# Kernel optimization log

Measured on AMD Instinct MI355X. Metric: run time of the kernel, lower is better.

The kernel has to match this reference:

```python
import jax, jax.numpy as jnp
import numpy as np

B, T, H = 2, 2048, 1024
I = 4096            # intermediate dim
HEADS = 4
RET = 128           # private expert retrieval dim
NUM_EXPERTS = 4096
NUM_KEYS = 64       # sqrt(NUM_EXPERTS)
K = 8               # num_cdmmoe_experts_per_head


def setup_inputs() -> dict:
    key = jax.random.key(0)
    ks = jax.random.split(key, 7)
    return {
        "hidden_states": jax.random.normal(ks[0], (B, T, H), jnp.float32),
        "W_up": jax.random.normal(ks[1], (I, H), jnp.float32) * 0.02,
        "W_down": jax.random.normal(ks[2], (H, I), jnp.float32) * 0.02,
        "W_q": jax.random.normal(ks[3], (HEADS * RET, H), jnp.float32) * 0.02,
        "keys": jax.random.normal(ks[4], (HEADS, NUM_KEYS, 2, RET // 2), jnp.float32) * 0.02,
        "down_embed": jax.random.normal(ks[5], (NUM_EXPERTS, H), jnp.float32) * 0.02,
        "up_embed": jax.random.normal(ks[6], (NUM_EXPERTS, H), jnp.float32) * 0.02,
    }


def reference(hidden_states, W_up, W_down, W_q, keys, down_embed, up_embed):
    b, t, hd = hidden_states.shape
    h, nk, _, n = keys.shape  # heads, num_keys, 2, half retrieval dim
    # queries: [b,t,h*2n] -> [2,b,t,h,n]
    q = jnp.einsum('btd,ed->bte', hidden_states, W_q)
    q = q.reshape(b, t, 2, h, n).transpose(2, 0, 1, 3, 4)
    # product-key similarities: [2,b,t,h,num_keys]
    sim = jnp.einsum('pbthn,hkpn->pbthk', q, keys)
    scores_xy, idx_xy = jax.lax.top_k(sim, K)  # [2,b,t,h,K]
    sx, sy = scores_xy[0], scores_xy[1]
    ix, iy = idx_xy[0], idx_xy[1]
    # cartesian combine: [b,t,h,K*K]
    all_scores = (sx[..., :, None] + sy[..., None, :]).reshape(b, t, h, K * K)
    all_idx = (ix[..., :, None] * nk + iy[..., None, :]).reshape(b, t, h, K * K)
    scores, pk = jax.lax.top_k(all_scores, K)               # [b,t,h,K]
    indices = jnp.take_along_axis(all_idx, pk, axis=-1)     # [b,t,h,K]
    de = down_embed[indices]  # [b,t,h,K,H]
    ue = up_embed[indices]    # [b,t,h,K,H]
    w = jax.nn.silu(jnp.einsum('btd,bthkd->bthk', hidden_states, de)
                    * jax.nn.softmax(scores, axis=-1))
    experts_states = jnp.einsum('bthk,bthkd->btd', w, ue)
    dense = jnp.einsum('bti,di->btd', jax.nn.silu(jnp.einsum('btd,id->bti', hidden_states, W_up)), W_down)
    return dense + experts_states
```

## Files before the change

### kernel.cpp

```cpp
#include <hip/hip_runtime.h>

typedef unsigned short u16;
typedef unsigned int u32;

#define TOKENS 4096
#define HDIM 1024
#define IDIM 4096
#define NHEADS 4
#define NKEYS 64
#define TOPK 8
#define QDIM 512

typedef __bf16 bf16x8 __attribute__((ext_vector_type(8)));
typedef float  f32x4  __attribute__((ext_vector_type(4)));
typedef u16    u16x8  __attribute__((ext_vector_type(8)));
typedef u32    u32x4  __attribute__((ext_vector_type(4)));

__device__ __forceinline__ u16 f2bf(float f) {
    u32 u = __float_as_uint(f);
    u += 0x7fffu + ((u >> 16) & 1u);
    return (u16)(u >> 16);
}
__device__ __forceinline__ float bf2f(u16 h) { return __uint_as_float(((u32)h) << 16); }

#define H_N4   1048576
#define WUP_N4 1048576
#define WDN_N4 1048576
#define DE_N4  1048576
#define UE_N4  1048576
#define CVT_TOT (H_N4 + WUP_N4)

__device__ __forceinline__ void cvt1(const float* in, u16* hi, u16* lo, int i) {
    float4 v = reinterpret_cast<const float4*>(in)[i];
    float vf[4] = {v.x, v.y, v.z, v.w};
    ushort4 h;
    u16 hh[4];
#pragma unroll
    for (int j = 0; j < 4; j++) hh[j] = f2bf(vf[j]);
    h.x = hh[0]; h.y = hh[1]; h.z = hh[2]; h.w = hh[3];
    reinterpret_cast<ushort4*>(hi)[i] = h;
    if (lo) {
        ushort4 l4;
        u16 ll[4];
#pragma unroll
        for (int j = 0; j < 4; j++) ll[j] = f2bf(vf[j] - bf2f(hh[j]));
        l4.x = ll[0]; l4.y = ll[1]; l4.z = ll[2]; l4.w = ll[3];
        reinterpret_cast<ushort4*>(lo)[i] = l4;
    }
}

__device__ __forceinline__ void cvt1_f8(const float* in, u32* out8, int i) {
    float4 v = reinterpret_cast<const float4*>(in)[i];
    u32 w = __builtin_amdgcn_cvt_pk_fp8_f32(v.x, v.y, 0u, false);
    w = __builtin_amdgcn_cvt_pk_fp8_f32(v.z, v.w, w, true);
    out8[i] = w;
}

__global__ __launch_bounds__(256) void cvt_all(
    const float* __restrict__ hidden, const float* __restrict__ W_up,
    u16* __restrict__ hid_hi, u16* __restrict__ hid_lo, u16* __restrict__ wup) {
    int i = blockIdx.x * 256 + threadIdx.x;
    if (i >= CVT_TOT) return;
    if (i < H_N4) { cvt1(hidden, hid_hi, hid_lo, i); return; }
    i -= H_N4;
    cvt1(W_up, wup, nullptr, i);
}

__global__ __launch_bounds__(256) void weff_kernel(
    const float* __restrict__ keys, const float* __restrict__ Wq,
    u16* __restrict__ weff_hi, u16* __restrict__ weff_lo) {
    __shared__ float kk[64][65];
    __shared__ float wq_s[64][128];

    const int g = blockIdx.x >> 3, ds = blockIdx.x & 7;
    const int p = g >> 2, h = g & 3;
    const int d0 = ds * 128;
    const int t = threadIdx.x;
    const int base = p * 256 + h * 64;

    {
        int k = t >> 2, part = t & 3;
        const float* krow = keys + (((size_t)(h * NKEYS + k) * 2 + p) * 64);
#pragma unroll
        for (int j = 0; j < 4; j++) {
            int n0 = part * 16 + j * 4;
            float4 v = *reinterpret_cast<const float4*>(krow + n0);
            kk[k][n0 + 0] = v.x; kk[k][n0 + 1] = v.y;
            kk[k][n0 + 2] = v.z; kk[k][n0 + 3] = v.w;
        }
    }
    {
        int n = t >> 2, dpart = t & 3;
        const float* wrow = Wq + (size_t)(base + n) * HDIM + d0;
#pragma unroll
        for (int j = 0; j < 8; j++) {
            int dd = dpart * 32 + j * 4;
            float4 v = *reinterpret_cast<const float4*>(wrow + dd);
            *reinterpret_cast<float4*>(&wq_s[n][dd]) = v;
        }
    }
    __syncthreads();

    const int k = t & 63, dq = t >> 6;
    float acc[32];
#pragma unroll
    for (int i = 0; i < 32; i++) acc[i] = 0.f;
    for (int n = 0; n < 64; n++) {
        float kv = kk[k][n];
        const float4* wrow = reinterpret_cast<const float4*>(&wq_s[n][dq * 32]);
#pragma unroll
        for (int j = 0; j < 8; j++) {
            float4 w4 = wrow[j];
            acc[j * 4 + 0] += kv * w4.x; acc[j * 4 + 1] += kv * w4.y;
            acc[j * 4 + 2] += kv * w4.z; acc[j * 4 + 3] += kv * w4.w;
        }
    }
    size_t ro = (size_t)(g * 64 + k) * HDIM + d0 + dq * 32;
#pragma unroll
    for (int j = 0; j < 8; j++) {
        ushort4 hh, ll;
        u16 hv[4], lv[4];
#pragma unroll
        for (int i = 0; i < 4; i++) {
            float a = acc[j * 4 + i];
            hv[i] = f2bf(a);
            lv[i] = f2bf(a - bf2f(hv[i]));
        }
        hh.x = hv[0]; hh.y = hv[1]; hh.z = hv[2]; hh.w = hv[3];
        ll.x = lv[0]; ll.y = lv[1]; ll.z = lv[2]; ll.w = lv[3];
        *reinterpret_cast<ushort4*>(weff_hi + ro + j * 4) = hh;
        *reinterpret_cast<ushort4*>(weff_lo + ro + j * 4) = ll;
    }
}

__global__ __launch_bounds__(256) void reduce_add4(float* __restrict__ out,
                                                   const float* __restrict__ p,
                                                   const float* __restrict__ ea,
                                                   const float* __restrict__ eb, int n4) {
    int i = blockIdx.x * 256 + threadIdx.x;
    if (i >= n4) return;
    float4 a = reinterpret_cast<const float4*>(out)[i];
    float4 b = reinterpret_cast<const float4*>(p)[i];
    float4 c = reinterpret_cast<const float4*>(ea)[i];
    float4 d = reinterpret_cast<const float4*>(eb)[i];
    a.x += b.x + c.x + d.x; a.y += b.y + c.y + d.y;
    a.z += b.z + c.z + d.z; a.w += b.w + c.w + d.w;
    reinterpret_cast<float4*>(out)[i] = a;
}

__device__ __forceinline__ void gload16(const void* g, void* s) {
    auto gp = reinterpret_cast<const __attribute__((address_space(1))) u32*>(
        reinterpret_cast<uintptr_t>(g));
    auto sp = reinterpret_cast<__attribute__((address_space(3))) u32*>(
        reinterpret_cast<uintptr_t>(s));
    __builtin_amdgcn_global_load_lds(gp, sp, 16, 0, 0);
}

#define BK 32

__device__ __forceinline__ int swz(int a) { return a ^ (((a >> 7) & 3) << 4); }

template <int ROWS, int THREADS>
__device__ __forceinline__ void stage_tile(const u16* g, size_t krow_b, size_t kb0,
                                           char* s, int t) {
#pragma unroll
    for (int rnd = 0; rnd < ROWS * 64 / (THREADS * 16); rnd++) {
        int o = t * 16 + rnd * THREADS * 16;
        int os = swz(o);
        int row = o >> 6, kb = os & 63;
        gload16((const char*)g + (size_t)row * krow_b + kb0 + kb, s + o);
    }
}

template <int N>
__device__ __forceinline__ void vm_wait() {
    if constexpr (N == 0) asm volatile("s_waitcnt vmcnt(0)" ::: "memory");
    else if constexpr (N == 3) asm volatile("s_waitcnt vmcnt(3)" ::: "memory");
    else if constexpr (N == 4) asm volatile("s_waitcnt vmcnt(4)" ::: "memory");
    else if constexpr (N == 6) asm volatile("s_waitcnt vmcnt(6)" ::: "memory");
    else if constexpr (N == 8) asm volatile("s_waitcnt vmcnt(8)" ::: "memory");
    else static_assert(N == 0, "unsupported vmcnt");
}

__device__ void up_body(char* smem, int bx, int by,
                        const u16* __restrict__ A, const u16* __restrict__ B,
                        u16* __restrict__ act, int M, int N, int K) {
    constexpr int LPS = 3;
    const int t = threadIdx.x;
    const int lane = t & 63;
    const int wave = t >> 6;
    const int wr = wave >> 1, wc = wave & 1;
    const int ro = lane & 15;
    const int ko = (lane >> 4) * 16;
    const int m0 = by * 256, n0 = bx * 128;

    f32x4 acc[4][4];
#pragma unroll
    for (int i = 0; i < 4; i++)
#pragma unroll
        for (int j = 0; j < 4; j++) acc[i][j] = (f32x4){0.f, 0.f, 0.f, 0.f};

    const size_t krow = (size_t)K * 2;
    const u16* Ab = A + (size_t)m0 * K;
    const u16* Bb = B + (size_t)n0 * K;
    char* smA = smem;
    char* smB = smem + 49152;

    auto stage_all = [&](int b, int k0) {
        size_t kb0 = (size_t)k0 * 2;
        stage_tile<256, 512>(Ab, krow, kb0, smA + b * 16384, t);
        stage_tile<128, 512>(Bb, krow, kb0, smB + b * 8192, t);
    };

    const int NU = K / BK;
    stage_all(0, 0);
    stage_all(1, BK);

    int cur = 0, pre = 2;
    for (int u = 0; u < NU; ++u) {
        if (u + 2 < NU) stage_all(pre, (u + 2) * BK);
        if (u + 2 < NU) vm_wait<2 * LPS>();
        else if (u + 1 < NU) vm_wait<LPS>();
        else vm_wait<0>();
        __builtin_amdgcn_s_barrier();

        const char* Ac = smA + cur * 16384;
        const char* Bc = smB + cur * 8192;
        bf16x8 fa[4], fb[4];
#pragma unroll
        for (int i = 0; i < 4; i++)
            fa[i] = *reinterpret_cast<const bf16x8*>(Ac + swz((wr * 64 + i * 16 + ro) * 64 + ko));
#pragma unroll
        for (int j = 0; j < 4; j++)
            fb[j] = *reinterpret_cast<const bf16x8*>(Bc + swz((wc * 64 + j * 16 + ro) * 64 + ko));
#pragma unroll
        for (int i = 0; i < 4; i++)
#pragma unroll
            for (int j = 0; j < 4; j++)
                acc[i][j] = __builtin_amdgcn_mfma_f32_16x16x32_bf16(fa[i], fb[j],
                                                                    acc[i][j], 0, 0, 0);
        __builtin_amdgcn_s_barrier();
        cur = (cur == 2) ? 0 : cur + 1;
        pre = (pre == 2) ? 0 : pre + 1;
    }

#pragma unroll
    for (int i = 0; i < 4; i++)
#pragma unroll
        for (int j = 0; j < 4; j++) {
            int col = n0 + wc * 64 + j * 16 + ro;
            int rbase = m0 + wr * 64 + i * 16 + (lane >> 4) * 4;
#pragma unroll
            for (int r = 0; r < 4; r++) {
                float v = acc[i][j][r];
                float s = v / (1.f + __expf(-v));
                act[(size_t)(rbase + r) * N + col] = f2bf(s);
            }
        }
}

__device__ void sim_body(char* smem, int bx, int by,
                         const u16* __restrict__ Ahi, const u16* __restrict__ Alo,
                         const u16* __restrict__ Bhi, const u16* __restrict__ Blo,
                         float* __restrict__ C, int M, int N, int K) {
    const int t = threadIdx.x;
    const int lane = t & 63;
    const int wave = t >> 6;
    const int wr = wave >> 2, wc = wave & 3;
    const int ro = lane & 15;
    const int ko = (lane >> 4) * 16;
    const int m0 = by * 64, n0 = bx * 128;

    f32x4 acc[2][2];
#pragma unroll
    for (int i = 0; i < 2; i++)
#pragma unroll
        for (int j = 0; j < 2; j++) acc[i][j] = (f32x4){0.f, 0.f, 0.f, 0.f};

    const size_t krow = (size_t)K * 2;
    const u16* Ahb = Ahi + (size_t)m0 * K;
    const u16* Alb = Alo + (size_t)m0 * K;
    const u16* Bhb = Bhi + (size_t)n0 * K;
    const u16* Blb = Blo + (size_t)n0 * K;
    char* smA = smem;
    char* smB = smem + 16384;

    auto stage_all = [&](int b, int k0) {
        size_t kb0 = (size_t)k0 * 2;
        {
            int sel = t >> 8, tt = t & 255;
            const u16* g = sel ? Alb : Ahb;
            int o = tt * 16;
            int os = swz(o);
            gload16((const char*)g + (size_t)(o >> 6) * krow + kb0 + (os & 63),
                    smA + b * 8192 + sel * 4096 + o);
        }
        {
            int o = t * 16, os = swz(o);
            gload16((const char*)Bhb + (size_t)(o >> 6) * krow + kb0 + (os & 63),
                    smB + b * 16384 + o);
        }
        {
            int o = t * 16, os = swz(o);
            gload16((const char*)Blb + (size_t)(o >> 6) * krow + kb0 + (os & 63),
                    smB + b * 16384 + 8192 + o);
        }
    };

    stage_all(0, 0);
    __syncthreads();
    int cur = 0;

    for (int k0 = 0; k0 < K; k0 += BK) {
        if (k0 + BK < K) stage_all(cur ^ 1, k0 + BK);
        const char* Ac = smA + cur * 8192;
        const char* Bc = smB + cur * 16384;
        bf16x8 fa[2], fal[2], fb[2], fbl[2];
#pragma unroll
        for (int i = 0; i < 2; i++) {
            int a = swz((wr * 32 + i * 16 + ro) * 64 + ko);
            fa[i] = *reinterpret_cast<const bf16x8*>(Ac + a);
            fal[i] = *reinterpret_cast<const bf16x8*>(Ac + 4096 + a);
        }
#pragma unroll
        for (int j = 0; j < 2; j++) {
            int a = swz((wc * 32 + j * 16 + ro) * 64 + ko);
            fb[j] = *reinterpret_cast<const bf16x8*>(Bc + a);
            fbl[j] = *reinterpret_cast<const bf16x8*>(Bc + 8192 + a);
        }
#pragma unroll
        for (int i = 0; i < 2; i++)
#pragma unroll
            for (int j = 0; j < 2; j++) {
                acc[i][j] = __builtin_amdgcn_mfma_f32_16x16x32_bf16(fa[i], fb[j],
                                                                    acc[i][j], 0, 0, 0);
                acc[i][j] = __builtin_amdgcn_mfma_f32_16x16x32_bf16(fa[i], fbl[j],
                                                                    acc[i][j], 0, 0, 0);
                acc[i][j] = __builtin_amdgcn_mfma_f32_16x16x32_bf16(fal[i], fb[j],
                                                                    acc[i][j], 0, 0, 0);
            }
        __syncthreads();
        cur ^= 1;
    }

#pragma unroll
    for (int i = 0; i < 2; i++)
#pragma unroll
        for (int j = 0; j < 2; j++) {
            int col = n0 + wc * 32 + j * 16 + ro;
            int rbase = m0 + wr * 32 + i * 16 + (lane >> 4) * 4;
#pragma unroll
            for (int r = 0; r < 4; r++)
                C[(size_t)(rbase + r) * N + col] = acc[i][j][r];
        }
}

__global__ __launch_bounds__(512, 4) void up_sim(
    const u16* __restrict__ hid_hi, const u16* __restrict__ hid_lo,
    const u16* __restrict__ wup,
    const u16* __restrict__ weff_hi, const u16* __restrict__ weff_lo,
    const float* __restrict__ W_down, const float* __restrict__ de,
    const float* __restrict__ ue,
    u16* __restrict__ act, float* __restrict__ Simb,
    u16* __restrict__ wdn, u32* __restrict__ de_f8, u32* __restrict__ ue_f8) {
    __shared__ char smem[73728];
    int bid = blockIdx.x;
    if (bid < 512) {
        int b2 = (bid & 7) * 64 + (bid >> 3);
        up_body(smem, b2 % 32, b2 / 32, hid_hi, wup, act, TOKENS, IDIM, HDIM);
    } else if (bid < 768) {
        int sb = bid - 512;
        sim_body(smem, sb & 3, sb >> 2, hid_hi, hid_lo, weff_hi, weff_lo, Simb,
                 TOKENS, QDIM, HDIM);
    } else {
        int idx = (bid - 768) * 512 + threadIdx.x;
#pragma unroll
        for (int j = 0; j < 24; j++) {
            int i = idx + j * 131072;
            if (i < WDN_N4) cvt1(W_down, wdn, nullptr, i);
            else if (i < WDN_N4 + DE_N4) cvt1_f8(de, de_f8, i - WDN_N4);
            else cvt1_f8(ue, ue_f8, i - WDN_N4 - DE_N4);
        }
    }
}

template <int TBM, int TBN, int WVM, int WVN, int KCHUNKS>
__global__ __launch_bounds__(WVM * WVN * 64) void gemm_p3(
    const u16* __restrict__ A, const u16* __restrict__ B,
    float* __restrict__ Cout, float* __restrict__ Cout2, int M, int N, int K) {
    constexpr int THREADS = WVM * WVN * 64;
    constexpr int WM = TBM / WVM, WN = TBN / WVN;
    constexpr int FM = WM / 16, FN = WN / 16;
    constexpr int LPS = (TBM + TBN) * 64 / (THREADS * 16);
    __shared__ u16 As[3][TBM * BK];
    __shared__ u16 Bs[3][TBN * BK];
    const int t = threadIdx.x;
    const int lane = t & 63;
    const int wave = t >> 6;
    const int wr = wave / WVN, wc = wave % WVN;
    const int ro = lane & 15;
    const int ko = (lane >> 4) * 16;

    int bx = blockIdx.x, by = blockIdx.y;
    {
        int gx = gridDim.x;
        int n = gx * gridDim.y;
        int bid = by * gx + bx;
        int q = n >> 3;
        bid = (bid & 7) * q + (bid >> 3);
        bx = bid % gx; by = bid / gx;
    }
    const int m0 = by * TBM;
    const int n0 = bx * TBN;
    const int klen = K / KCHUNKS;
    const int z = (KCHUNKS > 1) ? blockIdx.z : 0;
    const int koff = z * klen;
    const int NU = klen / BK;

    f32x4 acc[FM][FN];
#pragma unroll
    for (int i = 0; i < FM; i++)
#pragma unroll
        for (int j = 0; j < FN; j++) acc[i][j] = (f32x4){0.f, 0.f, 0.f, 0.f};

    const size_t krow = (size_t)K * 2;
    const u16* Ab = A + (size_t)m0 * K;
    const u16* Bb = B + (size_t)n0 * K;

    auto stage_all = [&](int b, int k0) {
        size_t kb0 = (size_t)k0 * 2;
        stage_tile<TBM, THREADS>(Ab, krow, kb0, (char*)As[b], t);
        stage_tile<TBN, THREADS>(Bb, krow, kb0, (char*)Bs[b], t);
    };

    stage_all(0, koff);
    stage_all(1, koff + BK);

    int cur = 0, pre = 2;
    for (int u = 0; u < NU; ++u) {
        int k0 = koff + u * BK;
        if (u + 2 < NU) stage_all(pre, k0 + 2 * BK);
        if (u + 2 < NU) vm_wait<2 * LPS>();
        else if (u + 1 < NU) vm_wait<LPS>();
        else vm_wait<0>();
        __builtin_amdgcn_s_barrier();

        const u16* Ac = As[cur];
        const u16* Bc = Bs[cur];
        bf16x8 fa[FM], fb[FN];
#pragma unroll
        for (int i = 0; i < FM; i++)
            fa[i] = *reinterpret_cast<const bf16x8*>(
                (const char*)Ac + swz((wr * WM + i * 16 + ro) * 64 + ko));
#pragma unroll
        for (int j = 0; j < FN; j++)
            fb[j] = *reinterpret_cast<const bf16x8*>(
                (const char*)Bc + swz((wc * WN + j * 16 + ro) * 64 + ko));
#pragma unroll
        for (int i = 0; i < FM; i++)
#pragma unroll
            for (int j = 0; j < FN; j++)
                acc[i][j] = __builtin_amdgcn_mfma_f32_16x16x32_bf16(fa[i], fb[j],
                                                                    acc[i][j], 0, 0, 0);
        __builtin_amdgcn_s_barrier();
        cur = (cur == 2) ? 0 : cur + 1;
        pre = (pre == 2) ? 0 : pre + 1;
    }

#pragma unroll
    for (int i = 0; i < FM; i++)
#pragma unroll
        for (int j = 0; j < FN; j++) {
            int col = n0 + wc * WN + j * 16 + ro;
            int rbase = m0 + wr * WM + i * 16 + (lane >> 4) * 4;
#pragma unroll
            for (int r = 0; r < 4; r++) {
                size_t off = (size_t)(rbase + r) * N + col;
                if (z == 0) Cout[off] = acc[i][j][r];
                else Cout2[off] = acc[i][j][r];
            }
        }
}

__device__ __forceinline__ int rank64(const float* base, float v, int l) {
    const float4* gv = reinterpret_cast<const float4*>(base);
    int rank = 0;
#pragma unroll
    for (int n = 0; n < 16; n++) {
        float4 o = gv[n];
        int b = n * 4;
        rank += (o.x > v) || (o.x == v && (b + 0) < l);
        rank += (o.y > v) || (o.y == v && (b + 1) < l);
        rank += (o.z > v) || (o.z == v && (b + 2) < l);
        rank += (o.w > v) || (o.w == v && (b + 3) < l);
    }
    return rank;
}

__global__ __launch_bounds__(256) void router_gather(
    const float* __restrict__ Simb, const u16* __restrict__ hid_bf,
    const u32* __restrict__ de_f8, const u32* __restrict__ ue_f8,
    float* __restrict__ expst_a, float* __restrict__ expst_b) {
    __shared__ float sims[QDIM];
    __shared__ float topv[8][TOPK];
    __shared__ int topi[8][TOPK];
    __shared__ float pv[NHEADS][64];
    __shared__ float st8[NHEADS][TOPK];
    __shared__ int sid8[NHEADS][TOPK];
    __shared__ float gate8[NHEADS][TOPK];
    __shared__ float wks_s[16];
    __shared__ int eids_s[16];

    const int tok = blockIdx.x >> 1;
    const int hf2 = blockIdx.x & 1;
    const int tid = threadIdx.x;
    const int w = tid >> 6, l = tid & 63;

    sims[tid] = Simb[(size_t)tok * QDIM + tid];
    sims[tid + 256] = Simb[(size_t)tok * QDIM + tid + 256];
    __syncthreads();

    {
#pragma unroll
        for (int rep = 0; rep < 2; rep++) {
            int g = w + rep * 4;
            float v = sims[g * 64 + l];
            int rank = rank64(sims + g * 64, v, l);
            if (rank < TOPK) { topv[g][rank] = v; topi[g][rank] = l; }
        }
    }
    __syncthreads();

    pv[w][l] = topv[w][l >> 3] + topv[4 + w][l & 7];
    __syncthreads();

    {
        float v = pv[w][l];
        int rank = rank64(pv[w], v, l);
        if (rank < TOPK) {
            st8[w][rank] = v;
            sid8[w][rank] = topi[w][l >> 3] * NKEYS + topi[4 + w][l & 7];
        }
    }
    __syncthreads();

    if (tid < NHEADS * TOPK) {
        int h = tid >> 3, r = tid & 7;
        float m0 = st8[h][0];
        float s = 0.f;
#pragma unroll
        for (int i = 0; i < TOPK; i++) s += __expf(st8[h][i] - m0);
        gate8[h][r] = __expf(st8[h][r] - m0) / s;
    }
    __syncthreads();

    {
        u16x8 hv[2];
        const u16* hrow = hid_bf + (size_t)tok * HDIM + l * 16;
        hv[0] = *reinterpret_cast<const u16x8*>(hrow);
        hv[1] = *reinterpret_cast<const u16x8*>(hrow + 8);
        float h16[16];
#pragma unroll
        for (int t2 = 0; t2 < 8; t2++) {
            h16[t2] = bf2f(hv[0][t2]);
            h16[8 + t2] = bf2f(hv[1][t2]);
        }
        int eid[4];
        float gt[4];
#pragma unroll
        for (int j = 0; j < 4; j++) {
            int i32 = hf2 * 16 + w * 4 + j;
            int h = i32 >> 3, k = i32 & 7;
            eid[j] = sid8[h][k];
            gt[j] = gate8[h][k];
        }
        u32x4 dv[4];
#pragma unroll
        for (int j = 0; j < 4; j++)
            dv[j] = *reinterpret_cast<const u32x4*>(de_f8 + (size_t)eid[j] * 256 + l * 4);
        float dot[4];
#pragma unroll
        for (int j = 0; j < 4; j++) {
            float s = 0.f;
#pragma unroll
            for (int w2 = 0; w2 < 4; w2++) {
                u32 word = dv[j][w2];
                s += h16[w2 * 4 + 0] * __builtin_amdgcn_cvt_f32_fp8(word, 0);
                s += h16[w2 * 4 + 1] * __builtin_amdgcn_cvt_f32_fp8(word, 1);
                s += h16[w2 * 4 + 2] * __builtin_amdgcn_cvt_f32_fp8(word, 2);
                s += h16[w2 * 4 + 3] * __builtin_amdgcn_cvt_f32_fp8(word, 3);
            }
            dot[j] = s;
        }
#pragma unroll
        for (int m = 32; m; m >>= 1)
#pragma unroll
            for (int j = 0; j < 4; j++) dot[j] += __shfl_xor(dot[j], m, 64);
        if (l < 4) {
            float x = dot[l] * gt[l];
            wks_s[w * 4 + l] = x / (1.f + __expf(-x));
            eids_s[w * 4 + l] = eid[l];
        }
    }
    __syncthreads();

    {
        float acc0 = 0.f, acc1 = 0.f, acc2 = 0.f, acc3 = 0.f;
        const u32* ubase = ue_f8 + w * 64 + l;
#pragma unroll
        for (int m = 0; m < 16; m++) {
            int e = eids_s[m];
            float wk = wks_s[m];
            u32 u = ubase[(size_t)e * 256];
            acc0 += wk * __builtin_amdgcn_cvt_f32_fp8(u, 0);
            acc1 += wk * __builtin_amdgcn_cvt_f32_fp8(u, 1);
            acc2 += wk * __builtin_amdgcn_cvt_f32_fp8(u, 2);
            acc3 += wk * __builtin_amdgcn_cvt_f32_fp8(u, 3);
        }
        float* dst = (hf2 == 0) ? expst_a : expst_b;
        *reinterpret_cast<float4*>(dst + (size_t)tok * HDIM + w * 256 + l * 4) =
            make_float4(acc0, acc1, acc2, acc3);
    }
}

extern "C" void kernel_launch(void* const* d_in, const int* in_sizes, int n_in,
                              void* d_out, int out_size, void* d_ws, size_t ws_size,
                              hipStream_t stream) {
    const float* hidden = (const float*)d_in[0];
    const float* W_up = (const float*)d_in[1];
    const float* W_down = (const float*)d_in[2];
    const float* W_q = (const float*)d_in[3];
    const float* keys = (const float*)d_in[4];
    const float* down_embed = (const float*)d_in[5];
    const float* up_embed = (const float*)d_in[6];
    float* out = (float*)d_out;

    char* ws = (char*)d_ws;
    size_t off = 0;
    auto alloc = [&](size_t bytes) {
        void* p = ws + off;
        off += (bytes + 255) & ~(size_t)255;
        return p;
    };
    u16* hid_hi = (u16*)alloc((size_t)TOKENS * HDIM * 2);
    u16* hid_lo = (u16*)alloc((size_t)TOKENS * HDIM * 2);
    float* Simb = (float*)alloc((size_t)TOKENS * QDIM * 4);
    float* partial = (float*)hid_lo;
    u16* weff_hi = (u16*)alloc((size_t)QDIM * HDIM * 2);
    u16* weff_lo = (u16*)alloc((size_t)QDIM * HDIM * 2);
    u16* wup = (u16*)alloc((size_t)IDIM * HDIM * 2);
    u16* wdn = (u16*)alloc((size_t)HDIM * IDIM * 2);
    u16* act = (u16*)alloc((size_t)TOKENS * IDIM * 2);
    u32* de_f8 = (u32*)alloc((size_t)4096 * HDIM);
    u32* ue_f8 = (u32*)alloc((size_t)4096 * HDIM);
    float* expst_a = (float*)alloc((size_t)TOKENS * HDIM * 4);
    float* expst_b = (float*)alloc((size_t)TOKENS * HDIM * 4);

    cvt_all<<<(CVT_TOT + 255) / 256, 256, 0, stream>>>(hidden, W_up, hid_hi, hid_lo, wup);
    weff_kernel<<<64, 256, 0, stream>>>(keys, W_q, weff_hi, weff_lo);

    up_sim<<<1024, 512, 0, stream>>>(hid_hi, hid_lo, wup, weff_hi, weff_lo,
                                     W_down, down_embed, up_embed,
                                     act, Simb, wdn, de_f8, ue_f8);

    router_gather<<<TOKENS * 2, 256, 0, stream>>>(Simb, hid_hi, de_f8, ue_f8,
                                                  expst_a, expst_b);

    gemm_p3<128, 128, 2, 2, 2>
        <<<dim3(HDIM / 128, TOKENS / 128, 2), 256, 0, stream>>>(
        act, wdn, out, partial, TOKENS, HDIM, IDIM);
    reduce_add4<<<(TOKENS * HDIM / 4 + 255) / 256, 256, 0, stream>>>(
        out, partial, expst_a, expst_b, TOKENS * HDIM / 4);
}
```

Before: 210.9 us.

## Move weight/embedding conversions into cvt_all and schedule sim blocks first

The W_down bf16 conversion and the fp8 conversions of the down/up expert embeddings move out of the fused up_sim launch and into the initial cvt_all kernel. up_sim now holds only the sim and up-projection GEMM blocks, with the sim blocks ordered first. The aim is to stop memory-bound conversion blocks from sharing the GEMM launch and to start the smaller sim work early. The trade-off is that these conversions no longer overlap with GEMM compute and instead lengthen the serial conversion kernel.

```diff
diff --git a/kernel.cpp b/kernel.cpp
--- a/kernel.cpp
+++ b/kernel.cpp
@@ -28,7 +28,7 @@
 #define WDN_N4 1048576
 #define DE_N4  1048576
 #define UE_N4  1048576
-#define CVT_TOT (H_N4 + WUP_N4)
+#define CVT_TOT (H_N4 + WUP_N4 + WDN_N4 + DE_N4 + UE_N4)
 
 __device__ __forceinline__ void cvt1(const float* in, u16* hi, u16* lo, int i) {
     float4 v = reinterpret_cast<const float4*>(in)[i];
@@ -58,12 +58,22 @@
 
 __global__ __launch_bounds__(256) void cvt_all(
     const float* __restrict__ hidden, const float* __restrict__ W_up,
-    u16* __restrict__ hid_hi, u16* __restrict__ hid_lo, u16* __restrict__ wup) {
+    const float* __restrict__ W_down, const float* __restrict__ de,
+    const float* __restrict__ ue,
+    u16* __restrict__ hid_hi, u16* __restrict__ hid_lo,
+    u16* __restrict__ wup, u16* __restrict__ wdn,
+    u32* __restrict__ de_f8, u32* __restrict__ ue_f8) {
     int i = blockIdx.x * 256 + threadIdx.x;
     if (i >= CVT_TOT) return;
     if (i < H_N4) { cvt1(hidden, hid_hi, hid_lo, i); return; }
     i -= H_N4;
-    cvt1(W_up, wup, nullptr, i);
+    if (i < WUP_N4) { cvt1(W_up, wup, nullptr, i); return; }
+    i -= WUP_N4;
+    if (i < WDN_N4) { cvt1(W_down, wdn, nullptr, i); return; }
+    i -= WDN_N4;
+    if (i < DE_N4) { cvt1_f8(de, de_f8, i); return; }
+    i -= DE_N4;
+    cvt1_f8(ue, ue_f8, i);
 }
 
 __global__ __launch_bounds__(256) void weff_kernel(
@@ -359,28 +369,17 @@
     const u16* __restrict__ hid_hi, const u16* __restrict__ hid_lo,
     const u16* __restrict__ wup,
     const u16* __restrict__ weff_hi, const u16* __restrict__ weff_lo,
-    const float* __restrict__ W_down, const float* __restrict__ de,
-    const float* __restrict__ ue,
-    u16* __restrict__ act, float* __restrict__ Simb,
-    u16* __restrict__ wdn, u32* __restrict__ de_f8, u32* __restrict__ ue_f8) {
+    u16* __restrict__ act, float* __restrict__ Simb) {
     __shared__ char smem[73728];
     int bid = blockIdx.x;
-    if (bid < 512) {
-        int b2 = (bid & 7) * 64 + (bid >> 3);
-        up_body(smem, b2 % 32, b2 / 32, hid_hi, wup, act, TOKENS, IDIM, HDIM);
-    } else if (bid < 768) {
-        int sb = bid - 512;
+    if (bid < 256) {
+        int sb = bid;
         sim_body(smem, sb & 3, sb >> 2, hid_hi, hid_lo, weff_hi, weff_lo, Simb,
                  TOKENS, QDIM, HDIM);
     } else {
-        int idx = (bid - 768) * 512 + threadIdx.x;
-#pragma unroll
-        for (int j = 0; j < 24; j++) {
-            int i = idx + j * 131072;
-            if (i < WDN_N4) cvt1(W_down, wdn, nullptr, i);
-            else if (i < WDN_N4 + DE_N4) cvt1_f8(de, de_f8, i - WDN_N4);
-            else cvt1_f8(ue, ue_f8, i - WDN_N4 - DE_N4);
-        }
+        int ub = bid - 256;
+        int b2 = (ub & 7) * 64 + (ub >> 3);
+        up_body(smem, b2 % 32, b2 / 32, hid_hi, wup, act, TOKENS, IDIM, HDIM);
     }
 }
 
@@ -656,12 +655,12 @@
     float* expst_a = (float*)alloc((size_t)TOKENS * HDIM * 4);
     float* expst_b = (float*)alloc((size_t)TOKENS * HDIM * 4);
 
-    cvt_all<<<(CVT_TOT + 255) / 256, 256, 0, stream>>>(hidden, W_up, hid_hi, hid_lo, wup);
+    cvt_all<<<(CVT_TOT + 255) / 256, 256, 0, stream>>>(
+        hidden, W_up, W_down, down_embed, up_embed,
+        hid_hi, hid_lo, wup, wdn, de_f8, ue_f8);
     weff_kernel<<<64, 256, 0, stream>>>(keys, W_q, weff_hi, weff_lo);
 
-    up_sim<<<1024, 512, 0, stream>>>(hid_hi, hid_lo, wup, weff_hi, weff_lo,
-                                     W_down, down_embed, up_embed,
-                                     act, Simb, wdn, de_f8, ue_f8);
+    up_sim<<<768, 512, 0, stream>>>(hid_hi, hid_lo, wup, weff_hi, weff_lo, act, Simb);
 
     router_gather<<<TOKENS * 2, 256, 0, stream>>>(Simb, hid_hi, de_f8, ue_f8,
                                                   expst_a, expst_b);
```

Result: no change. 212.6 us (+0.8%).
